# Kernel optimization log

Hardware: AMD Instinct MI355X
Metric: run time of the kernel (lower is better)

Reference implementation:

```python
import jax, jax.numpy as jnp
import numpy as np

B, T, H, K, NL = 64, 1024, 256, 64, 2  # batch, seq, n_hidden, n_tensors, n_layers
U = 2 * K  # GRU units


def _unif(key, shape):
    return jax.random.uniform(key, shape, jnp.float32, -0.2, 0.2)


def setup_inputs() -> dict:
    key = jax.random.key(0)
    ks = jax.random.split(key, 16)
    return {
        "x": jax.random.normal(ks[0], (B, T, H), jnp.float32),
        "m0_a": _unif(ks[1], (1, H)),
        "m0_o": _unif(ks[2], (1, H)),
        "Ua": _unif(ks[3], (K, H, H)),
        "Uo": _unif(ks[4], (K, H, H)),
        "Va": _unif(ks[5], (K, H, H)),
        "Vo": _unif(ks[6], (K, H, H)),
        "Ma": _unif(ks[7], (H, H)),
        "Mo": _unif(ks[8], (H, H)),
        "va": _unif(ks[9], (U, 1)),
        "vo": _unif(ks[10], (U, 1)),
        "Wa": _unif(ks[11], (U, 3 * U)),  # GRU kernel (z|r|h), input dim = U
        "Ra": _unif(ks[12], (U, 3 * U)),  # GRU recurrent kernel
        "Wo": _unif(ks[13], (U, 3 * U)),
        "Ro": _unif(ks[14], (U, 3 * U)),
    }


def gru_seq(seq, W, R):
    # Keras GRU, reset_after=True, use_bias=False, recurrent_activation=sigmoid.
    # seq: [B, T, U] -> [B, T, U]
    units = R.shape[0]
    xW = seq @ W  # [B, T, 3U] precomputed input projections

    def step(h, xw_t):
        xz, xr, xh = jnp.split(xw_t, 3, axis=-1)
        hz, hr, hc = jnp.split(h @ R, 3, axis=-1)
        z = jax.nn.sigmoid(xz + hz)
        r = jax.nn.sigmoid(xr + hr)
        hh = jnp.tanh(xh + r * hc)
        hn = z * h + (1.0 - z) * hh
        return hn, hn

    h0 = jnp.zeros((seq.shape[0], units), seq.dtype)
    _, ys = jax.lax.scan(step, h0, jnp.swapaxes(xW, 0, 1))
    return jnp.swapaxes(ys, 0, 1)


def cmla_forward(x, m0_a, m0_o, Ua, Uo, Va, Vo, Ma, Mo, va, vo, Wa, Ra, Wo, Ro):
    b = x.shape[0]
    ma = jnp.broadcast_to(m0_a, (b, m0_a.shape[-1]))  # [B, H]
    mo = jnp.broadcast_to(m0_o, (b, m0_o.shape[-1]))
    asp_sum = jnp.zeros((b, x.shape[1], U), x.dtype)
    opi_sum = jnp.zeros((b, x.shape[1], U), x.dtype)
    for i in range(NL):
        # tensor products: [K,H,H] x [B,H] -> [B,K,H]; then [B,T,H] x [B,K,H] -> [B,T,K]
        a1 = jnp.einsum('bth,bkh->btk', x, jnp.einsum('khj,bj->bkh', Ua, ma))
        a2 = jnp.einsum('bth,bkh->btk', x, jnp.einsum('khj,bj->bkh', Va, mo))
        o1 = jnp.einsum('bth,bkh->btk', x, jnp.einsum('khj,bj->bkh', Uo, ma))
        o2 = jnp.einsum('bth,bkh->btk', x, jnp.einsum('khj,bj->bkh', Vo, mo))
        aspect = jnp.tanh(jnp.concatenate([a1, a2], axis=-1))   # [B,T,2K]
        opinion = jnp.tanh(jnp.concatenate([o1, o2], axis=-1))  # [B,T,2K]
        ra = gru_seq(aspect, Wa, Ra)
        ro = gru_seq(opinion, Wo, Ro)
        asp_sum = asp_sum + ra
        opi_sum = opi_sum + ro
        if i < NL - 1:
            alpha_a = jax.nn.softmax(jnp.einsum('btu,u->bt', ra, va[:, 0]), axis=-1)
            alpha_o = jax.nn.softmax(jnp.einsum('btu,u->bt', ro, vo[:, 0]), axis=-1)
            ctx_a = jnp.einsum('bt,bth->bh', alpha_a, x)  # attention-pooled context
            ctx_o = jnp.einsum('bt,bth->bh', alpha_o, x)
            ma = jnp.tanh(ma @ Ma) + ctx_a
            mo = jnp.tanh(mo @ Mo) + ctx_o
    return asp_sum, opi_sum


def reference(x, m0_a, m0_o, Ua, Uo, Va, Vo, Ma, Mo, va, vo, Wa, Ra, Wo, Ro):
    return cmla_forward(x, m0_a, m0_o, Ua, Uo, Va, Vo, Ma, Mo, va, vo, Wa, Ra, Wo, Ro)
```

## Files before the change

kernel.cpp:

```cpp
#include <hip/hip_runtime.h>
#include <hip/hip_bf16.h>
#include <math.h>

#define B_  64
#define T_  1024
#define H_  256
#define K_  64
#define U_  128
#define U3_ 384

#define LOG2E_F 1.4426950408889634f

typedef unsigned short ushort_t;
typedef __attribute__((ext_vector_type(8))) short short8;
typedef __attribute__((ext_vector_type(8))) _Float16 half8;
typedef __attribute__((ext_vector_type(4))) _Float16 half4v;
typedef __attribute__((ext_vector_type(4))) float floatx4;

__device__ __forceinline__ float bf2f(ushort_t v) {
  unsigned int u = ((unsigned int)v) << 16;
  return __builtin_bit_cast(float, u);
}
__device__ __forceinline__ float h2f(ushort_t v) {
  return (float)__builtin_bit_cast(_Float16, v);
}
__device__ __forceinline__ ushort_t f2h(float f) {
  return __builtin_bit_cast(ushort_t, (_Float16)f);
}
__device__ __forceinline__ float ldf(const void* p, size_t i, int isf) {
  return isf ? ((const float*)p)[i] : bf2f(((const ushort_t*)p)[i]);
}
__device__ __forceinline__ float exp2_hw(float x) {
  float r;
  asm volatile("v_exp_f32 %0, %1\n\ts_nop 0" : "=v"(r) : "v"(x));
  return r;
}
__device__ __forceinline__ unsigned pk2h(float a, float b) {
  unsigned r;
  asm("v_cvt_pkrtz_f16_f32 %0, %1, %2" : "=v"(r) : "v"(a), "v"(b));
  return r;
}
__device__ __forceinline__ float tanh_fast(float x) {
  float E = exp2_hw(2.f * LOG2E_F * x);
  return 1.f - 2.f * __builtin_amdgcn_rcpf(E + 1.f);
}

__global__ void k_sniff(const ushort_t* __restrict__ xr, int* __restrict__ flag) {
  __shared__ int red[256];
  int tx = threadIdx.x;
  int hits = 0;
  for (int i = 0; i < 64; ++i) {
    ushort_t w = xr[tx + i * 256];
    int e = (w >> 7) & 0xff;
    hits += (e >= 0x70 && e <= 0x82) ? 1 : 0;
  }
  red[tx] = hits;
  __syncthreads();
  for (int off = 128; off > 0; off >>= 1) {
    if (tx < off) red[tx] += red[tx + off];
    __syncthreads();
  }
  if (tx == 0) flag[0] = (red[0] < 12288) ? 1 : 0;
}

__global__ __launch_bounds__(256) void k_canon_x(const void* __restrict__ xr,
                                                 const int* __restrict__ flag,
                                                 ushort_t* __restrict__ x16) {
  int tid = blockIdx.x * 256 + threadIdx.x;
  float v[8];
  if (*flag) {
    const float4* xf = (const float4*)xr;
    float4 a = xf[tid * 2], b = xf[tid * 2 + 1];
    v[0] = a.x; v[1] = a.y; v[2] = a.z; v[3] = a.w;
    v[4] = b.x; v[5] = b.y; v[6] = b.z; v[7] = b.w;
  } else {
    uint4 raw = ((const uint4*)xr)[tid];
    v[0] = bf2f((ushort_t)(raw.x & 0xffff)); v[1] = bf2f((ushort_t)(raw.x >> 16));
    v[2] = bf2f((ushort_t)(raw.y & 0xffff)); v[3] = bf2f((ushort_t)(raw.y >> 16));
    v[4] = bf2f((ushort_t)(raw.z & 0xffff)); v[5] = bf2f((ushort_t)(raw.z >> 16));
    v[6] = bf2f((ushort_t)(raw.w & 0xffff)); v[7] = bf2f((ushort_t)(raw.w >> 16));
  }
  uint4 o;
  o.x = (unsigned)f2h(v[0]) | ((unsigned)f2h(v[1]) << 16);
  o.y = (unsigned)f2h(v[2]) | ((unsigned)f2h(v[3]) << 16);
  o.z = (unsigned)f2h(v[4]) | ((unsigned)f2h(v[5]) << 16);
  o.w = (unsigned)f2h(v[6]) | ((unsigned)f2h(v[7]) << 16);
  ((uint4*)x16)[tid] = o;
}

__global__ void k_init_m(const void* __restrict__ m0a, const void* __restrict__ m0o,
                         const int* __restrict__ flag,
                         float* __restrict__ ma_ws, float* __restrict__ mo_ws) {
  int b = blockIdx.x, tx = threadIdx.x, isf = *flag;
  ma_ws[b * H_ + tx] = ldf(m0a, tx, isf);
  mo_ws[b * H_ + tx] = ldf(m0o, tx, isf);
}

__global__ void k_transpose(const void* __restrict__ Wa, const void* __restrict__ Wo,
                            const int* __restrict__ flag, ushort_t* __restrict__ Wt16) {
  int bx = blockIdx.x, isf = *flag;
  int g = bx / 192;
  int i = (bx % 192) * 256 + threadIdx.x;
  const void* W = g ? Wo : Wa;
  int jj = i >> 7, u = i & 127;
  float sc = (jj < 256) ? -LOG2E_F : (2.f * LOG2E_F);
  Wt16[(size_t)g * (U3_ * U_) + i] = f2h(ldf(W, u * U3_ + jj, isf) * sc);
}

__global__ __launch_bounds__(256) void k_phaseA(
    const void* __restrict__ Ua, const void* __restrict__ Va,
    const void* __restrict__ Uo, const void* __restrict__ Vo,
    const int* __restrict__ flag,
    const float* __restrict__ ma_ws, const float* __restrict__ mo_ws,
    ushort_t* __restrict__ P16) {
  int gk = blockIdx.x;
  int g = gk >> 6, k = gk & 63;
  const void* U = (g == 0) ? Ua : (g == 1) ? Va : (g == 2) ? Uo : Vo;
  const float* msrc = (g & 1) ? mo_ws : ma_ws;
  int tx = threadIdx.x;
  int isf = *flag;
  __shared__ __align__(16) float m_l[64 * 128];
  float acc[64];
#pragma unroll
  for (int b = 0; b < 64; ++b) acc[b] = 0.f;
  size_t rowoff = ((size_t)k * H_ + tx) * H_;
  for (int pass = 0; pass < 2; ++pass) {
    for (int i = 0; i < 32; ++i) {
      int flat = tx + i * 256;
      m_l[flat] = msrc[(flat >> 7) * H_ + pass * 128 + (flat & 127)];
    }
    __syncthreads();
    for (int c = 0; c < 16; ++c) {
      float uv[8];
      if (isf) {
        const float* uf = (const float*)U + rowoff + pass * 128 + c * 8;
        float4 A = *(const float4*)uf;
        float4 Bv = *(const float4*)(uf + 4);
        uv[0] = A.x; uv[1] = A.y; uv[2] = A.z; uv[3] = A.w;
        uv[4] = Bv.x; uv[5] = Bv.y; uv[6] = Bv.z; uv[7] = Bv.w;
      } else {
        const ushort_t* ub = (const ushort_t*)U + rowoff + pass * 128 + c * 8;
        uint4 raw = *(const uint4*)ub;
        uv[0] = bf2f((ushort_t)(raw.x & 0xffff)); uv[1] = bf2f((ushort_t)(raw.x >> 16));
        uv[2] = bf2f((ushort_t)(raw.y & 0xffff)); uv[3] = bf2f((ushort_t)(raw.y >> 16));
        uv[4] = bf2f((ushort_t)(raw.z & 0xffff)); uv[5] = bf2f((ushort_t)(raw.z >> 16));
        uv[6] = bf2f((ushort_t)(raw.w & 0xffff)); uv[7] = bf2f((ushort_t)(raw.w >> 16));
      }
#pragma unroll
      for (int b = 0; b < 64; ++b) {
        const float* mr = &m_l[b * 128 + c * 8];
        float4 mA = *(const float4*)mr;
        float4 mB = *(const float4*)(mr + 4);
        float s = acc[b];
        s = fmaf(uv[0], mA.x, s); s = fmaf(uv[1], mA.y, s);
        s = fmaf(uv[2], mA.z, s); s = fmaf(uv[3], mA.w, s);
        s = fmaf(uv[4], mB.x, s); s = fmaf(uv[5], mB.y, s);
        s = fmaf(uv[6], mB.z, s); s = fmaf(uv[7], mB.w, s);
        acc[b] = s;
      }
    }
    __syncthreads();
  }
  size_t base = ((size_t)(g * 64 + k)) * H_ + tx;
#pragma unroll 4
  for (int b = 0; b < 64; ++b) P16[base + (size_t)b * (256 * H_)] = f2h(acc[b]);
}

__global__ __launch_bounds__(256) void k_phaseB(
    const ushort_t* __restrict__ x16, const ushort_t* __restrict__ P16,
    ushort_t* __restrict__ aspect, ushort_t* __restrict__ opinion) {
  int bx = blockIdx.x;
  int b = bx >> 6, tt = bx & 63;
  int w = threadIdx.x >> 6;
  int lane = threadIdx.x & 63;
  int m = lane & 15, q = lane >> 4;
  const ushort_t* arow = x16 + ((size_t)(b * T_ + tt * 16 + m)) * H_ + q * 8;
  half8 af[8];
#pragma unroll
  for (int c = 0; c < 8; ++c)
    af[c] = __builtin_bit_cast(half8, *(const short8*)(arow + c * 32));
  const ushort_t* pbase = P16 + ((size_t)(b * 256 + m)) * H_ + q * 8;
#pragma unroll
  for (int s = 0; s < 4; ++s) {
    int ntile = s * 4 + w;
    const ushort_t* brow = pbase + (size_t)(ntile * 16) * H_;
    floatx4 acc = {0.f, 0.f, 0.f, 0.f}, acc2 = acc;
#pragma unroll
    for (int c = 0; c < 4; ++c) {
      half8 bf = __builtin_bit_cast(half8, *(const short8*)(brow + c * 32));
      acc = __builtin_amdgcn_mfma_f32_16x16x32_f16(af[c], bf, acc, 0, 0, 0);
      half8 bf2 = __builtin_bit_cast(half8, *(const short8*)(brow + (c + 4) * 32));
      acc2 = __builtin_amdgcn_mfma_f32_16x16x32_f16(af[c + 4], bf2, acc2, 0, 0, 0);
    }
    int n = ntile * 16 + m;
    ushort_t* dst;
    int nn;
    if (n < 128) { dst = aspect; nn = n; } else { dst = opinion; nn = n - 128; }
#pragma unroll
    for (int i = 0; i < 4; ++i) {
      int t = tt * 16 + q * 4 + i;
      dst[((size_t)(b * T_ + t)) * U_ + nn] = f2h(tanh_fast(acc[i] + acc2[i]));
    }
  }
}

__global__ __launch_bounds__(256) void k_phaseC(
    const ushort_t* __restrict__ aspect, const ushort_t* __restrict__ opinion,
    const ushort_t* __restrict__ Wt16,
    ushort_t* __restrict__ zr_a, ushort_t* __restrict__ zr_o,
    ushort_t* __restrict__ xh_a, ushort_t* __restrict__ xh_o) {
  int g = blockIdx.y;
  const ushort_t* A = g ? opinion : aspect;
  const ushort_t* Bm = Wt16 + (size_t)g * (U3_ * U_);
  ushort_t* ZR = g ? zr_o : zr_a;
  ushort_t* XH = g ? xh_o : xh_a;
  int mt = blockIdx.x;
  int w = threadIdx.x >> 6;
  int lane = threadIdx.x & 63;
  int m = lane & 15, q = lane >> 4;
  const ushort_t* arow = A + ((size_t)(mt * 16 + m)) * U_ + q * 8;
  half8 af[4];
#pragma unroll
  for (int c = 0; c < 4; ++c)
    af[c] = __builtin_bit_cast(half8, *(const short8*)(arow + c * 32));
  const ushort_t* bbase = Bm + (size_t)m * U_ + q * 8;
#pragma unroll
  for (int s = 0; s < 6; ++s) {
    int nt = s * 4 + w;
    const ushort_t* brow = bbase + (size_t)(nt * 16) * U_;
    floatx4 acc = {0.f, 0.f, 0.f, 0.f};
#pragma unroll
    for (int c = 0; c < 4; ++c) {
      half8 bf = __builtin_bit_cast(half8, *(const short8*)(brow + c * 32));
      acc = __builtin_amdgcn_mfma_f32_16x16x32_f16(af[c], bf, acc, 0, 0, 0);
    }
    int col = nt * 16 + m;
    if (nt < 16) {
      int c2 = (col < 128) ? (((col >> 2) << 3) + (col & 3))
                           : ((((col - 128) >> 2) << 3) + 4 + (col & 3));
#pragma unroll
      for (int i = 0; i < 4; ++i) {
        int row = mt * 16 + q * 4 + i;
        ZR[(size_t)row * 256 + c2] = f2h(acc[i]);
      }
    } else {
#pragma unroll
      for (int i = 0; i < 4; ++i) {
        int row = mt * 16 + q * 4 + i;
        XH[(size_t)row * U_ + (col - 256)] = f2h(acc[i]);
      }
    }
  }
}

template <int LAYER>
__global__ __launch_bounds__(512) void k_scan(
    const ushort_t* __restrict__ zr_a, const ushort_t* __restrict__ zr_o,
    const ushort_t* __restrict__ xh_a, const ushort_t* __restrict__ xh_o,
    const ushort_t* __restrict__ Rt16,
    float* __restrict__ out) {
  int g = blockIdx.x >> 2;
  int bb = (blockIdx.x & 3) << 4;
  int tid = threadIdx.x;
  int w = tid >> 6;
  int lane = tid & 63;
  int r = lane & 15;
  int q = lane >> 4;
  int b = bb + r;
  int j = (w << 4) + (q << 2);

  const ushort_t* zr = g ? zr_o : zr_a;
  const ushort_t* xh = g ? xh_o : xh_a;
  const ushort_t* Rt = Rt16 + (size_t)g * (U3_ * U_);

  half8 af[3][4];
#pragma unroll
  for (int gt = 0; gt < 3; ++gt) {
    size_t row = (size_t)(128 * gt + 16 * w + r) * U_;
#pragma unroll
    for (int ks = 0; ks < 4; ++ks)
      af[gt][ks] = __builtin_bit_cast(half8, *(const short8*)(Rt + row + ks * 32 + q * 8));
  }

  __shared__ __align__(16) ushort_t hbuf[4096];
  ((uint2*)hbuf)[tid] = (uint2){0u, 0u};

  float hs0 = 0.f, hs1 = 0.f, hs2 = 0.f, hs3 = 0.f;

  const ushort_t* zp = zr + (size_t)b * (T_ * 256) + ((j >> 2) << 3);
  const ushort_t* xp = xh + (size_t)b * (T_ * U_) + j;
  float* op = out + ((size_t)g * B_ * T_ + (size_t)b * T_) * U_ + j;

  uint4 zrA = *(const uint4*)zp;
  uint4 zrB = *(const uint4*)(zp + 256);
  uint2 hA = *(const uint2*)xp;
  uint2 hB = *(const uint2*)(xp + U_);
  float4 oA = make_float4(0.f, 0.f, 0.f, 0.f), oB = oA;
  if (LAYER) {
    oA = *(const float4*)op;
    oB = *(const float4*)(op + U_);
  }
  float4 pendE = make_float4(0.f, 0.f, 0.f, 0.f), pendO = pendE;

  int wofs = (w >> 1) * 512 + (r + 16 * (((w & 1) << 1) + (q >> 1))) * 8 + (q & 1) * 4;

  __syncthreads();

  for (int t = 0; t < T_; t += 2) {
    {
      half8 bf0 = __builtin_bit_cast(half8, *(const short8*)(&hbuf[0 * 512 + lane * 8]));
      half8 bf1 = __builtin_bit_cast(half8, *(const short8*)(&hbuf[1 * 512 + lane * 8]));
      half8 bf2 = __builtin_bit_cast(half8, *(const short8*)(&hbuf[2 * 512 + lane * 8]));
      half8 bf3 = __builtin_bit_cast(half8, *(const short8*)(&hbuf[3 * 512 + lane * 8]));
      if (t != 0) *(float4*)(op - U_) = pendO;
      int adv = (t + 2 < T_) ? 2 : 0;
      uint4 pzr = *(const uint4*)(zp + adv * 256);
      uint2 ph = *(const uint2*)(xp + adv * U_);
      float4 po;
      if (LAYER) po = *(const float4*)(op + adv * U_);

      floatx4 a0 = {0.f, 0.f, 0.f, 0.f}, a1 = a0, a2 = a0, c0 = a0, c1 = a0, c2 = a0;
      a0 = __builtin_amdgcn_mfma_f32_16x16x32_f16(af[0][0], bf0, a0, 0, 0, 0);
      a1 = __builtin_amdgcn_mfma_f32_16x16x32_f16(af[1][0], bf0, a1, 0, 0, 0);
      a2 = __builtin_amdgcn_mfma_f32_16x16x32_f16(af[2][0], bf0, a2, 0, 0, 0);
      c0 = __builtin_amdgcn_mfma_f32_16x16x32_f16(af[0][2], bf2, c0, 0, 0, 0);
      c1 = __builtin_amdgcn_mfma_f32_16x16x32_f16(af[1][2], bf2, c1, 0, 0, 0);
      c2 = __builtin_amdgcn_mfma_f32_16x16x32_f16(af[2][2], bf2, c2, 0, 0, 0);
      a0 = __builtin_amdgcn_mfma_f32_16x16x32_f16(af[0][1], bf1, a0, 0, 0, 0);
      a1 = __builtin_amdgcn_mfma_f32_16x16x32_f16(af[1][1], bf1, a1, 0, 0, 0);
      a2 = __builtin_amdgcn_mfma_f32_16x16x32_f16(af[2][1], bf1, a2, 0, 0, 0);
      c0 = __builtin_amdgcn_mfma_f32_16x16x32_f16(af[0][3], bf3, c0, 0, 0, 0);
      c1 = __builtin_amdgcn_mfma_f32_16x16x32_f16(af[1][3], bf3, c1, 0, 0, 0);
      c2 = __builtin_amdgcn_mfma_f32_16x16x32_f16(af[2][3], bf3, c2, 0, 0, 0);

      half8 zr8 = __builtin_bit_cast(half8, zrA);
      half4v xh4 = __builtin_bit_cast(half4v, hA);
      float hp[4] = {hs0, hs1, hs2, hs3};
      float hn[4];
#pragma unroll
      for (int i = 0; i < 4; ++i) {
        float zq = (float)zr8[i] + (a0[i] + c0[i]);
        float rq = (float)zr8[4 + i] + (a1[i] + c1[i]);
        float z = __builtin_amdgcn_rcpf(1.f + exp2_hw(zq));
        float rr = __builtin_amdgcn_rcpf(1.f + exp2_hw(rq));
        float y2 = fmaf(rr, a2[i] + c2[i], (float)xh4[i]);
        float th = fmaf(-2.f, __builtin_amdgcn_rcpf(exp2_hw(y2) + 1.f), 1.f);
        hn[i] = fmaf(z, hp[i] - th, th);
      }
      hs0 = hn[0]; hs1 = hn[1]; hs2 = hn[2]; hs3 = hn[3];
      pendE.x = LAYER ? (oA.x + hn[0]) : hn[0];
      pendE.y = LAYER ? (oA.y + hn[1]) : hn[1];
      pendE.z = LAYER ? (oA.z + hn[2]) : hn[2];
      pendE.w = LAYER ? (oA.w + hn[3]) : hn[3];
      uint2 wv;
      wv.x = pk2h(hn[0], hn[1]);
      wv.y = pk2h(hn[2], hn[3]);
      *(uint2*)(&hbuf[2048 + wofs]) = wv;
      zrA = pzr; hA = ph;
      if (LAYER) oA = po;
    }
    asm volatile("s_waitcnt lgkmcnt(0)" ::: "memory");
    __builtin_amdgcn_s_barrier();
    __builtin_amdgcn_sched_barrier(0);
    {
      half8 bf0 = __builtin_bit_cast(half8, *(const short8*)(&hbuf[2048 + 0 * 512 + lane * 8]));
      half8 bf1 = __builtin_bit_cast(half8, *(const short8*)(&hbuf[2048 + 1 * 512 + lane * 8]));
      half8 bf2 = __builtin_bit_cast(half8, *(const short8*)(&hbuf[2048 + 2 * 512 + lane * 8]));
      half8 bf3 = __builtin_bit_cast(half8, *(const short8*)(&hbuf[2048 + 3 * 512 + lane * 8]));
      *(float4*)op = pendE;
      int adv = (t + 3 < T_) ? 2 : 0;
      uint4 pzr = *(const uint4*)(zp + 256 + adv * 256);
      uint2 ph = *(const uint2*)(xp + U_ + adv * U_);
      float4 po;
      if (LAYER) po = *(const float4*)(op + U_ + adv * U_);

      floatx4 a0 = {0.f, 0.f, 0.f, 0.f}, a1 = a0, a2 = a0, c0 = a0, c1 = a0, c2 = a0;
      a0 = __builtin_amdgcn_mfma_f32_16x16x32_f16(af[0][0], bf0, a0, 0, 0, 0);
      a1 = __builtin_amdgcn_mfma_f32_16x16x32_f16(af[1][0], bf0, a1, 0, 0, 0);
      a2 = __builtin_amdgcn_mfma_f32_16x16x32_f16(af[2][0], bf0, a2, 0, 0, 0);
      c0 = __builtin_amdgcn_mfma_f32_16x16x32_f16(af[0][2], bf2, c0, 0, 0, 0);
      c1 = __builtin_amdgcn_mfma_f32_16x16x32_f16(af[1][2], bf2, c1, 0, 0, 0);
      c2 = __builtin_amdgcn_mfma_f32_16x16x32_f16(af[2][2], bf2, c2, 0, 0, 0);
      a0 = __builtin_amdgcn_mfma_f32_16x16x32_f16(af[0][1], bf1, a0, 0, 0, 0);
      a1 = __builtin_amdgcn_mfma_f32_16x16x32_f16(af[1][1], bf1, a1, 0, 0, 0);
      a2 = __builtin_amdgcn_mfma_f32_16x16x32_f16(af[2][1], bf1, a2, 0, 0, 0);
      c0 = __builtin_amdgcn_mfma_f32_16x16x32_f16(af[0][3], bf3, c0, 0, 0, 0);
      c1 = __builtin_amdgcn_mfma_f32_16x16x32_f16(af[1][3], bf3, c1, 0, 0, 0);
      c2 = __builtin_amdgcn_mfma_f32_16x16x32_f16(af[2][3], bf3, c2, 0, 0, 0);

      half8 zr8 = __builtin_bit_cast(half8, zrB);
      half4v xh4 = __builtin_bit_cast(half4v, hB);
      float hp[4] = {hs0, hs1, hs2, hs3};
      float hn[4];
#pragma unroll
      for (int i = 0; i < 4; ++i) {
        float zq = (float)zr8[i] + (a0[i] + c0[i]);
        float rq = (float)zr8[4 + i] + (a1[i] + c1[i]);
        float z = __builtin_amdgcn_rcpf(1.f + exp2_hw(zq));
        float rr = __builtin_amdgcn_rcpf(1.f + exp2_hw(rq));
        float y2 = fmaf(rr, a2[i] + c2[i], (float)xh4[i]);
        float th = fmaf(-2.f, __builtin_amdgcn_rcpf(exp2_hw(y2) + 1.f), 1.f);
        hn[i] = fmaf(z, hp[i] - th, th);
      }
      hs0 = hn[0]; hs1 = hn[1]; hs2 = hn[2]; hs3 = hn[3];
      pendO.x = LAYER ? (oB.x + hn[0]) : hn[0];
      pendO.y = LAYER ? (oB.y + hn[1]) : hn[1];
      pendO.z = LAYER ? (oB.z + hn[2]) : hn[2];
      pendO.w = LAYER ? (oB.w + hn[3]) : hn[3];
      uint2 wv;
      wv.x = pk2h(hn[0], hn[1]);
      wv.y = pk2h(hn[2], hn[3]);
      *(uint2*)(&hbuf[0 + wofs]) = wv;
      zrB = pzr; hB = ph;
      if (LAYER) oB = po;
    }
    asm volatile("s_waitcnt lgkmcnt(0)" ::: "memory");
    __builtin_amdgcn_s_barrier();
    __builtin_amdgcn_sched_barrier(0);
    zp += 512; xp += 2 * U_; op += 2 * U_;
  }
  *(float4*)(op - U_) = pendO;
}

__global__ void k_score(const float* __restrict__ out, const void* __restrict__ va,
                        const void* __restrict__ vo, const int* __restrict__ flag,
                        float* __restrict__ scores) {
  int wave = threadIdx.x >> 6, lane = threadIdx.x & 63;
  int pair = blockIdx.x * 4 + wave;
  int g = pair >> 16;
  int bt = pair & 65535;
  int isf = *flag;
  const void* v = g ? vo : va;
  const float* o = out + ((size_t)g * (B_ * T_) + bt) * U_ + lane * 2;
  float s = o[0] * ldf(v, lane * 2, isf) + o[1] * ldf(v, lane * 2 + 1, isf);
#pragma unroll
  for (int off = 32; off > 0; off >>= 1) s += __shfl_down(s, off, 64);
  if (lane == 0) scores[pair] = s;
}

__global__ void k_softmax(float* __restrict__ scores) {
  int row = blockIdx.x;
  float* s = scores + (size_t)row * T_;
  int tx = threadIdx.x;
  __shared__ float red[256];
  float v[4];
  float mx = -1e30f;
#pragma unroll
  for (int i = 0; i < 4; ++i) { v[i] = s[tx + i * 256]; mx = fmaxf(mx, v[i]); }
  red[tx] = mx;
  __syncthreads();
  for (int off = 128; off > 0; off >>= 1) {
    if (tx < off) red[tx] = fmaxf(red[tx], red[tx + off]);
    __syncthreads();
  }
  float M = red[0];
  __syncthreads();
  float sm = 0.f;
#pragma unroll
  for (int i = 0; i < 4; ++i) { v[i] = expf(v[i] - M); sm += v[i]; }
  red[tx] = sm;
  __syncthreads();
  for (int off = 128; off > 0; off >>= 1) {
    if (tx < off) red[tx] += red[tx + off];
    __syncthreads();
  }
  float inv = 1.f / red[0];
#pragma unroll
  for (int i = 0; i < 4; ++i) s[tx + i * 256] = v[i] * inv;
}

__global__ __launch_bounds__(1024) void k_ctx_m(const float* __restrict__ alpha,
                                                const void* __restrict__ x,
                                                const void* __restrict__ Ma,
                                                const void* __restrict__ Mo,
                                                const int* __restrict__ flag,
                                                float* __restrict__ ma_ws,
                                                float* __restrict__ mo_ws) {
  int g = blockIdx.x >> 6, b = blockIdx.x & 63;
  int isf = *flag;
  int tid = threadIdx.x;
  int tx = tid & 255;
  int ty = tid >> 8;
  __shared__ float a_l[1024];
  __shared__ float m_l[256];
  __shared__ float pA[4][256];
  __shared__ float pB[4][256];
  const float* al = alpha + ((size_t)g * B_ + b) * T_;
  a_l[tid] = al[tid];
  if (ty == 0) m_l[tx] = (g ? mo_ws : ma_ws)[b * H_ + tx];
  __syncthreads();
  const void* Mm = g ? Mo : Ma;
  float acc = 0.f;
#pragma unroll 4
  for (int t0 = 0; t0 < 256; ++t0) {
    int t = ty * 256 + t0;
    acc = fmaf(a_l[t], ldf(x, (size_t)(b * T_ + t) * H_ + tx, isf), acc);
  }
  float acc2 = 0.f;
#pragma unroll 4
  for (int c = 0; c < 64; ++c) {
    int jj = ty * 64 + c;
    acc2 = fmaf(m_l[jj], ldf(Mm, (size_t)jj * 256 + tx, isf), acc2);
  }
  pA[ty][tx] = acc;
  pB[ty][tx] = acc2;
  __syncthreads();
  if (ty == 0) {
    float A = pA[0][tx] + pA[1][tx] + pA[2][tx] + pA[3][tx];
    float Bv = pB[0][tx] + pB[1][tx] + pB[2][tx] + pB[3][tx];
    float* m_ws = g ? mo_ws : ma_ws;
    m_ws[b * H_ + tx] = tanhf(Bv) + A;
  }
}

extern "C" void kernel_launch(void* const* d_in, const int* in_sizes, int n_in,
                              void* d_out, int out_size, void* d_ws, size_t ws_size,
                              hipStream_t stream) {
  const void* x_r = d_in[0];
  const void* m0a = d_in[1];
  const void* m0o = d_in[2];
  const void* Ua  = d_in[3];
  const void* Uo  = d_in[4];
  const void* Va  = d_in[5];
  const void* Vo  = d_in[6];
  const void* Ma  = d_in[7];
  const void* Mo  = d_in[8];
  const void* va  = d_in[9];
  const void* vo  = d_in[10];
  const void* Wa  = d_in[11];
  const void* Ra  = d_in[12];
  const void* Wo  = d_in[13];
  const void* Ro  = d_in[14];
  float* out = (float*)d_out;

  char* ws = (char*)d_ws;
  int*      flag    = (int*)(ws + 0);
  float*    ma_ws   = (float*)(ws + 1024);
  float*    mo_ws   = (float*)(ws + 66560);
  ushort_t* Wt16    = (ushort_t*)(ws + 132096);
  ushort_t* x16     = (ushort_t*)(ws + 328704);
  ushort_t* P16     = (ushort_t*)(ws + 33883136);
  float*    scores  = (float*)(ws + 33883136);
  ushort_t* Rt16    = (ushort_t*)(ws + 33883136 + 1048576);
  ushort_t* aspect  = (ushort_t*)(ws + 42271744);
  ushort_t* opinion = (ushort_t*)(ws + 59048960);
  ushort_t* zr_a    = (ushort_t*)(ws + 75826176);
  ushort_t* zr_o    = (ushort_t*)(ws + 109380608);
  ushort_t* xh_a    = (ushort_t*)(ws + 142935040);
  ushort_t* xh_o    = (ushort_t*)(ws + 159712256);

  if (ws_size < 176489472ULL) return;

  k_sniff<<<dim3(1), dim3(256), 0, stream>>>((const ushort_t*)x_r, flag);
  k_canon_x<<<dim3(8192), dim3(256), 0, stream>>>(x_r, flag, x16);
  k_init_m<<<dim3(64), dim3(256), 0, stream>>>(m0a, m0o, flag, ma_ws, mo_ws);
  k_transpose<<<dim3(384), dim3(256), 0, stream>>>(Wa, Wo, flag, Wt16);

  for (int layer = 0; layer < 2; ++layer) {
    k_phaseA<<<dim3(256), dim3(256), 0, stream>>>(Ua, Va, Uo, Vo, flag, ma_ws, mo_ws, P16);
    k_phaseB<<<dim3(4096), dim3(256), 0, stream>>>(x16, P16, aspect, opinion);
    k_phaseC<<<dim3(4096, 2), dim3(256), 0, stream>>>(aspect, opinion, Wt16, zr_a, zr_o, xh_a, xh_o);
    k_transpose<<<dim3(384), dim3(256), 0, stream>>>(Ra, Ro, flag, Rt16);
    if (layer == 0) {
      k_scan<0><<<dim3(8), dim3(512), 0, stream>>>(zr_a, zr_o, xh_a, xh_o, Rt16, out);
      k_score<<<dim3(32768), dim3(256), 0, stream>>>(out, va, vo, flag, scores);
      k_softmax<<<dim3(128), dim3(256), 0, stream>>>(scores);
      k_ctx_m<<<dim3(128), dim3(1024), 0, stream>>>(scores, x_r, Ma, Mo, flag, ma_ws, mo_ws);
    } else {
      k_scan<1><<<dim3(8), dim3(512), 0, stream>>>(zr_a, zr_o, xh_a, xh_o, Rt16, out);
    }
  }
}
```

Baseline: 2.492 ms.

## Halve scan block to four waves, each computing two column groups

The GRU scan kernel now runs with 256 threads (4 waves) per block instead of 512. Each wave handles two 16-column groups of the hidden state, holding twice the recurrent-weight fragments in registers. The idea is to cut barrier cost and cross-wave synchronisation per timestep, in exchange for more serial MFMA and gate work per wave. The MFMA accumulation is now chained fully through K instead of split into two partial sums, which lengthens the dependency chain per output.

```diff
diff --git a/kernel.cpp b/kernel.cpp
--- a/kernel.cpp
+++ b/kernel.cpp
@@ -43,6 +43,32 @@
 __device__ __forceinline__ float tanh_fast(float x) {
   float E = exp2_hw(2.f * LOG2E_F * x);
   return 1.f - 2.f * __builtin_amdgcn_rcpf(E + 1.f);
+}
+
+__device__ __forceinline__ void gru_gate4(floatx4 az, floatx4 ar, floatx4 ah,
+                                          uint4 zrv, uint2 hv, float4 ov,
+                                          float* hs, float4& pend, uint2& wv,
+                                          int addold) {
+  half8 zr8 = __builtin_bit_cast(half8, zrv);
+  half4v xh4 = __builtin_bit_cast(half4v, hv);
+  float hn[4];
+#pragma unroll
+  for (int i = 0; i < 4; ++i) {
+    float zq = (float)zr8[i] + az[i];
+    float rq = (float)zr8[4 + i] + ar[i];
+    float z = __builtin_amdgcn_rcpf(1.f + exp2_hw(zq));
+    float rr = __builtin_amdgcn_rcpf(1.f + exp2_hw(rq));
+    float y2 = fmaf(rr, ah[i], (float)xh4[i]);
+    float th = fmaf(-2.f, __builtin_amdgcn_rcpf(exp2_hw(y2) + 1.f), 1.f);
+    hn[i] = fmaf(z, hs[i] - th, th);
+    hs[i] = hn[i];
+  }
+  pend.x = addold ? (ov.x + hn[0]) : hn[0];
+  pend.y = addold ? (ov.y + hn[1]) : hn[1];
+  pend.z = addold ? (ov.z + hn[2]) : hn[2];
+  pend.w = addold ? (ov.w + hn[3]) : hn[3];
+  wv.x = pk2h(hn[0], hn[1]);
+  wv.y = pk2h(hn[2], hn[3]);
 }
 
 __global__ void k_sniff(const ushort_t* __restrict__ xr, int* __restrict__ flag) {
@@ -254,7 +280,7 @@
 }
 
 template <int LAYER>
-__global__ __launch_bounds__(512) void k_scan(
+__global__ __launch_bounds__(256, 1) void k_scan(
     const ushort_t* __restrict__ zr_a, const ushort_t* __restrict__ zr_o,
     const ushort_t* __restrict__ xh_a, const ushort_t* __restrict__ xh_o,
     const ushort_t* __restrict__ Rt16,
@@ -267,42 +293,50 @@
   int r = lane & 15;
   int q = lane >> 4;
   int b = bb + r;
-  int j = (w << 4) + (q << 2);
+  int j0 = (w << 4) + (q << 2);
 
   const ushort_t* zr = g ? zr_o : zr_a;
   const ushort_t* xh = g ? xh_o : xh_a;
   const ushort_t* Rt = Rt16 + (size_t)g * (U3_ * U_);
 
-  half8 af[3][4];
-#pragma unroll
-  for (int gt = 0; gt < 3; ++gt) {
-    size_t row = (size_t)(128 * gt + 16 * w + r) * U_;
-#pragma unroll
-    for (int ks = 0; ks < 4; ++ks)
-      af[gt][ks] = __builtin_bit_cast(half8, *(const short8*)(Rt + row + ks * 32 + q * 8));
-  }
+  half8 af[2][3][4];
+#pragma unroll
+  for (int jg = 0; jg < 2; ++jg)
+#pragma unroll
+    for (int gt = 0; gt < 3; ++gt) {
+      size_t row = (size_t)(128 * gt + 64 * jg + 16 * w + r) * U_;
+#pragma unroll
+      for (int ks = 0; ks < 4; ++ks)
+        af[jg][gt][ks] =
+            __builtin_bit_cast(half8, *(const short8*)(Rt + row + ks * 32 + q * 8));
+    }
 
   __shared__ __align__(16) ushort_t hbuf[4096];
-  ((uint2*)hbuf)[tid] = (uint2){0u, 0u};
-
-  float hs0 = 0.f, hs1 = 0.f, hs2 = 0.f, hs3 = 0.f;
-
-  const ushort_t* zp = zr + (size_t)b * (T_ * 256) + ((j >> 2) << 3);
-  const ushort_t* xp = xh + (size_t)b * (T_ * U_) + j;
-  float* op = out + ((size_t)g * B_ * T_ + (size_t)b * T_) * U_ + j;
-
-  uint4 zrA = *(const uint4*)zp;
-  uint4 zrB = *(const uint4*)(zp + 256);
-  uint2 hA = *(const uint2*)xp;
-  uint2 hB = *(const uint2*)(xp + U_);
-  float4 oA = make_float4(0.f, 0.f, 0.f, 0.f), oB = oA;
+  ((uint4*)hbuf)[tid] = (uint4){0u, 0u, 0u, 0u};
+
+  float hs0[4] = {0.f, 0.f, 0.f, 0.f};
+  float hs1[4] = {0.f, 0.f, 0.f, 0.f};
+
+  const ushort_t* zp = zr + (size_t)b * (T_ * 256) + j0 * 2;
+  const ushort_t* xp = xh + (size_t)b * (T_ * U_) + j0;
+  float* op = out + ((size_t)g * B_ * T_ + (size_t)b * T_) * U_ + j0;
+
+  uint4 zrA0 = *(const uint4*)zp;
+  uint4 zrA1 = *(const uint4*)(zp + 128);
+  uint4 zrB0 = *(const uint4*)(zp + 256);
+  uint4 zrB1 = *(const uint4*)(zp + 256 + 128);
+  uint2 hA0 = *(const uint2*)xp;
+  uint2 hA1 = *(const uint2*)(xp + 64);
+  uint2 hB0 = *(const uint2*)(xp + U_);
+  uint2 hB1 = *(const uint2*)(xp + U_ + 64);
+  float4 oA0 = make_float4(0.f, 0.f, 0.f, 0.f), oA1 = oA0, oB0 = oA0, oB1 = oA0;
   if (LAYER) {
-    oA = *(const float4*)op;
-    oB = *(const float4*)(op + U_);
-  }
-  float4 pendE = make_float4(0.f, 0.f, 0.f, 0.f), pendO = pendE;
-
-  int wofs = (w >> 1) * 512 + (r + 16 * (((w & 1) << 1) + (q >> 1))) * 8 + (q & 1) * 4;
+    oA0 = *(const float4*)op;            oA1 = *(const float4*)(op + 64);
+    oB0 = *(const float4*)(op + U_);     oB1 = *(const float4*)(op + U_ + 64);
+  }
+  float4 pendE0, pendE1, pendO0, pendO1;
+
+  int wof0 = ((j0 >> 5) << 9) + (((j0 >> 3) & 3) << 7) + (r << 3) + (j0 & 7);
 
   __syncthreads();
 
@@ -312,52 +346,52 @@
       half8 bf1 = __builtin_bit_cast(half8, *(const short8*)(&hbuf[1 * 512 + lane * 8]));
       half8 bf2 = __builtin_bit_cast(half8, *(const short8*)(&hbuf[2 * 512 + lane * 8]));
       half8 bf3 = __builtin_bit_cast(half8, *(const short8*)(&hbuf[3 * 512 + lane * 8]));
-      if (t != 0) *(float4*)(op - U_) = pendO;
+      if (t != 0) {
+        *(float4*)(op - U_) = pendO0;
+        *(float4*)(op - U_ + 64) = pendO1;
+      }
       int adv = (t + 2 < T_) ? 2 : 0;
-      uint4 pzr = *(const uint4*)(zp + adv * 256);
-      uint2 ph = *(const uint2*)(xp + adv * U_);
-      float4 po;
-      if (LAYER) po = *(const float4*)(op + adv * U_);
-
-      floatx4 a0 = {0.f, 0.f, 0.f, 0.f}, a1 = a0, a2 = a0, c0 = a0, c1 = a0, c2 = a0;
-      a0 = __builtin_amdgcn_mfma_f32_16x16x32_f16(af[0][0], bf0, a0, 0, 0, 0);
-      a1 = __builtin_amdgcn_mfma_f32_16x16x32_f16(af[1][0], bf0, a1, 0, 0, 0);
-      a2 = __builtin_amdgcn_mfma_f32_16x16x32_f16(af[2][0], bf0, a2, 0, 0, 0);
-      c0 = __builtin_amdgcn_mfma_f32_16x16x32_f16(af[0][2], bf2, c0, 0, 0, 0);
-      c1 = __builtin_amdgcn_mfma_f32_16x16x32_f16(af[1][2], bf2, c1, 0, 0, 0);
-      c2 = __builtin_amdgcn_mfma_f32_16x16x32_f16(af[2][2], bf2, c2, 0, 0, 0);
-      a0 = __builtin_amdgcn_mfma_f32_16x16x32_f16(af[0][1], bf1, a0, 0, 0, 0);
-      a1 = __builtin_amdgcn_mfma_f32_16x16x32_f16(af[1][1], bf1, a1, 0, 0, 0);
-      a2 = __builtin_amdgcn_mfma_f32_16x16x32_f16(af[2][1], bf1, a2, 0, 0, 0);
-      c0 = __builtin_amdgcn_mfma_f32_16x16x32_f16(af[0][3], bf3, c0, 0, 0, 0);
-      c1 = __builtin_amdgcn_mfma_f32_16x16x32_f16(af[1][3], bf3, c1, 0, 0, 0);
-      c2 = __builtin_amdgcn_mfma_f32_16x16x32_f16(af[2][3], bf3, c2, 0, 0, 0);
-
-      half8 zr8 = __builtin_bit_cast(half8, zrA);
-      half4v xh4 = __builtin_bit_cast(half4v, hA);
-      float hp[4] = {hs0, hs1, hs2, hs3};
-      float hn[4];
-#pragma unroll
-      for (int i = 0; i < 4; ++i) {
-        float zq = (float)zr8[i] + (a0[i] + c0[i]);
-        float rq = (float)zr8[4 + i] + (a1[i] + c1[i]);
-        float z = __builtin_amdgcn_rcpf(1.f + exp2_hw(zq));
-        float rr = __builtin_amdgcn_rcpf(1.f + exp2_hw(rq));
-        float y2 = fmaf(rr, a2[i] + c2[i], (float)xh4[i]);
-        float th = fmaf(-2.f, __builtin_amdgcn_rcpf(exp2_hw(y2) + 1.f), 1.f);
-        hn[i] = fmaf(z, hp[i] - th, th);
+      uint4 pz0 = *(const uint4*)(zp + adv * 256);
+      uint4 pz1 = *(const uint4*)(zp + adv * 256 + 128);
+      uint2 ph0 = *(const uint2*)(xp + adv * U_);
+      uint2 ph1 = *(const uint2*)(xp + adv * U_ + 64);
+      float4 po0, po1;
+      if (LAYER) {
+        po0 = *(const float4*)(op + adv * U_);
+        po1 = *(const float4*)(op + adv * U_ + 64);
       }
-      hs0 = hn[0]; hs1 = hn[1]; hs2 = hn[2]; hs3 = hn[3];
-      pendE.x = LAYER ? (oA.x + hn[0]) : hn[0];
-      pendE.y = LAYER ? (oA.y + hn[1]) : hn[1];
-      pendE.z = LAYER ? (oA.z + hn[2]) : hn[2];
-      pendE.w = LAYER ? (oA.w + hn[3]) : hn[3];
-      uint2 wv;
-      wv.x = pk2h(hn[0], hn[1]);
-      wv.y = pk2h(hn[2], hn[3]);
-      *(uint2*)(&hbuf[2048 + wofs]) = wv;
-      zrA = pzr; hA = ph;
-      if (LAYER) oA = po;
+      floatx4 zz = {0.f, 0.f, 0.f, 0.f};
+      floatx4 az0 = __builtin_amdgcn_mfma_f32_16x16x32_f16(af[0][0][0], bf0,
+                    __builtin_amdgcn_mfma_f32_16x16x32_f16(af[0][0][1], bf1,
+                    __builtin_amdgcn_mfma_f32_16x16x32_f16(af[0][0][2], bf2,
+                    __builtin_amdgcn_mfma_f32_16x16x32_f16(af[0][0][3], bf3, zz, 0,0,0), 0,0,0), 0,0,0), 0,0,0);
+      floatx4 ar0 = __builtin_amdgcn_mfma_f32_16x16x32_f16(af[0][1][0], bf0,
+                    __builtin_amdgcn_mfma_f32_16x16x32_f16(af[0][1][1], bf1,
+                    __builtin_amdgcn_mfma_f32_16x16x32_f16(af[0][1][2], bf2,
+                    __builtin_amdgcn_mfma_f32_16x16x32_f16(af[0][1][3], bf3, zz, 0,0,0), 0,0,0), 0,0,0), 0,0,0);
+      floatx4 ah0 = __builtin_amdgcn_mfma_f32_16x16x32_f16(af[0][2][0], bf0,
+                    __builtin_amdgcn_mfma_f32_16x16x32_f16(af[0][2][1], bf1,
+                    __builtin_amdgcn_mfma_f32_16x16x32_f16(af[0][2][2], bf2,
+                    __builtin_amdgcn_mfma_f32_16x16x32_f16(af[0][2][3], bf3, zz, 0,0,0), 0,0,0), 0,0,0), 0,0,0);
+      floatx4 az1 = __builtin_amdgcn_mfma_f32_16x16x32_f16(af[1][0][0], bf0,
+                    __builtin_amdgcn_mfma_f32_16x16x32_f16(af[1][0][1], bf1,
+                    __builtin_amdgcn_mfma_f32_16x16x32_f16(af[1][0][2], bf2,
+                    __builtin_amdgcn_mfma_f32_16x16x32_f16(af[1][0][3], bf3, zz, 0,0,0), 0,0,0), 0,0,0), 0,0,0);
+      floatx4 ar1 = __builtin_amdgcn_mfma_f32_16x16x32_f16(af[1][1][0], bf0,
+                    __builtin_amdgcn_mfma_f32_16x16x32_f16(af[1][1][1], bf1,
+                    __builtin_amdgcn_mfma_f32_16x16x32_f16(af[1][1][2], bf2,
+                    __builtin_amdgcn_mfma_f32_16x16x32_f16(af[1][1][3], bf3, zz, 0,0,0), 0,0,0), 0,0,0), 0,0,0);
+      floatx4 ah1 = __builtin_amdgcn_mfma_f32_16x16x32_f16(af[1][2][0], bf0,
+                    __builtin_amdgcn_mfma_f32_16x16x32_f16(af[1][2][1], bf1,
+                    __builtin_amdgcn_mfma_f32_16x16x32_f16(af[1][2][2], bf2,
+                    __builtin_amdgcn_mfma_f32_16x16x32_f16(af[1][2][3], bf3, zz, 0,0,0), 0,0,0), 0,0,0), 0,0,0);
+      uint2 wv0, wv1;
+      gru_gate4(az0, ar0, ah0, zrA0, hA0, oA0, hs0, pendE0, wv0, LAYER);
+      gru_gate4(az1, ar1, ah1, zrA1, hA1, oA1, hs1, pendE1, wv1, LAYER);
+      *(uint2*)(&hbuf[2048 + wof0]) = wv0;
+      *(uint2*)(&hbuf[2048 + 1024 + wof0]) = wv1;
+      zrA0 = pz0; zrA1 = pz1; hA0 = ph0; hA1 = ph1;
+      if (LAYER) { oA0 = po0; oA1 = po1; }
     }
     asm volatile("s_waitcnt lgkmcnt(0)" ::: "memory");
     __builtin_amdgcn_s_barrier();
@@ -367,59 +401,58 @@
       half8 bf1 = __builtin_bit_cast(half8, *(const short8*)(&hbuf[2048 + 1 * 512 + lane * 8]));
       half8 bf2 = __builtin_bit_cast(half8, *(const short8*)(&hbuf[2048 + 2 * 512 + lane * 8]));
       half8 bf3 = __builtin_bit_cast(half8, *(const short8*)(&hbuf[2048 + 3 * 512 + lane * 8]));
-      *(float4*)op = pendE;
+      *(float4*)op = pendE0;
+      *(float4*)(op + 64) = pendE1;
       int adv = (t + 3 < T_) ? 2 : 0;
-      uint4 pzr = *(const uint4*)(zp + 256 + adv * 256);
-      uint2 ph = *(const uint2*)(xp + U_ + adv * U_);
-      float4 po;
-      if (LAYER) po = *(const float4*)(op + U_ + adv * U_);
-
-      floatx4 a0 = {0.f, 0.f, 0.f, 0.f}, a1 = a0, a2 = a0, c0 = a0, c1 = a0, c2 = a0;
-      a0 = __builtin_amdgcn_mfma_f32_16x16x32_f16(af[0][0], bf0, a0, 0, 0, 0);
-      a1 = __builtin_amdgcn_mfma_f32_16x16x32_f16(af[1][0], bf0, a1, 0, 0, 0);
-      a2 = __builtin_amdgcn_mfma_f32_16x16x32_f16(af[2][0], bf0, a2, 0, 0, 0);
-      c0 = __builtin_amdgcn_mfma_f32_16x16x32_f16(af[0][2], bf2, c0, 0, 0, 0);
-      c1 = __builtin_amdgcn_mfma_f32_16x16x32_f16(af[1][2], bf2, c1, 0, 0, 0);
-      c2 = __builtin_amdgcn_mfma_f32_16x16x32_f16(af[2][2], bf2, c2, 0, 0, 0);
-      a0 = __builtin_amdgcn_mfma_f32_16x16x32_f16(af[0][1], bf1, a0, 0, 0, 0);
-      a1 = __builtin_amdgcn_mfma_f32_16x16x32_f16(af[1][1], bf1, a1, 0, 0, 0);
-      a2 = __builtin_amdgcn_mfma_f32_16x16x32_f16(af[2][1], bf1, a2, 0, 0, 0);
-      c0 = __builtin_amdgcn_mfma_f32_16x16x32_f16(af[0][3], bf3, c0, 0, 0, 0);
-      c1 = __builtin_amdgcn_mfma_f32_16x16x32_f16(af[1][3], bf3, c1, 0, 0, 0);
-      c2 = __builtin_amdgcn_mfma_f32_16x16x32_f16(af[2][3], bf3, c2, 0, 0, 0);
-
-      half8 zr8 = __builtin_bit_cast(half8, zrB);
-      half4v xh4 = __builtin_bit_cast(half4v, hB);
-      float hp[4] = {hs0, hs1, hs2, hs3};
-      float hn[4];
-#pragma unroll
-      for (int i = 0; i < 4; ++i) {
-        float zq = (float)zr8[i] + (a0[i] + c0[i]);
-        float rq = (float)zr8[4 + i] + (a1[i] + c1[i]);
-        float z = __builtin_amdgcn_rcpf(1.f + exp2_hw(zq));
-        float rr = __builtin_amdgcn_rcpf(1.f + exp2_hw(rq));
-        float y2 = fmaf(rr, a2[i] + c2[i], (float)xh4[i]);
-        float th = fmaf(-2.f, __builtin_amdgcn_rcpf(exp2_hw(y2) + 1.f), 1.f);
-        hn[i] = fmaf(z, hp[i] - th, th);
+      uint4 pz0 = *(const uint4*)(zp + 256 + adv * 256);
+      uint4 pz1 = *(const uint4*)(zp + 256 + adv * 256 + 128);
+      uint2 ph0 = *(const uint2*)(xp + U_ + adv * U_);
+      uint2 ph1 = *(const uint2*)(xp + U_ + adv * U_ + 64);
+      float4 po0, po1;
+      if (LAYER) {
+        po0 = *(const float4*)(op + U_ + adv * U_);
+        po1 = *(const float4*)(op + U_ + adv * U_ + 64);
       }
-      hs0 = hn[0]; hs1 = hn[1]; hs2 = hn[2]; hs3 = hn[3];
-      pendO.x = LAYER ? (oB.x + hn[0]) : hn[0];
-      pendO.y = LAYER ? (oB.y + hn[1]) : hn[1];
-      pendO.z = LAYER ? (oB.z + hn[2]) : hn[2];
-      pendO.w = LAYER ? (oB.w + hn[3]) : hn[3];
-      uint2 wv;
-      wv.x = pk2h(hn[0], hn[1]);
-      wv.y = pk2h(hn[2], hn[3]);
-      *(uint2*)(&hbuf[0 + wofs]) = wv;
-      zrB = pzr; hB = ph;
-      if (LAYER) oB = po;
+      floatx4 zz = {0.f, 0.f, 0.f, 0.f};
+      floatx4 az0 = __builtin_amdgcn_mfma_f32_16x16x32_f16(af[0][0][0], bf0,
+                    __builtin_amdgcn_mfma_f32_16x16x32_f16(af[0][0][1], bf1,
+                    __builtin_amdgcn_mfma_f32_16x16x32_f16(af[0][0][2], bf2,
+                    __builtin_amdgcn_mfma_f32_16x16x32_f16(af[0][0][3], bf3, zz, 0,0,0), 0,0,0), 0,0,0), 0,0,0);
+      floatx4 ar0 = __builtin_amdgcn_mfma_f32_16x16x32_f16(af[0][1][0], bf0,
+                    __builtin_amdgcn_mfma_f32_16x16x32_f16(af[0][1][1], bf1,
+                    __builtin_amdgcn_mfma_f32_16x16x32_f16(af[0][1][2], bf2,
+                    __builtin_amdgcn_mfma_f32_16x16x32_f16(af[0][1][3], bf3, zz, 0,0,0), 0,0,0), 0,0,0), 0,0,0);
+      floatx4 ah0 = __builtin_amdgcn_mfma_f32_16x16x32_f16(af[0][2][0], bf0,
+                    __builtin_amdgcn_mfma_f32_16x16x32_f16(af[0][2][1], bf1,
+                    __builtin_amdgcn_mfma_f32_16x16x32_f16(af[0][2][2], bf2,
+                    __builtin_amdgcn_mfma_f32_16x16x32_f16(af[0][2][3], bf3, zz, 0,0,0), 0,0,0), 0,0,0), 0,0,0);
+      floatx4 az1 = __builtin_amdgcn_mfma_f32_16x16x32_f16(af[1][0][0], bf0,
+                    __builtin_amdgcn_mfma_f32_16x16x32_f16(af[1][0][1], bf1,
+                    __builtin_amdgcn_mfma_f32_16x16x32_f16(af[1][0][2], bf2,
+                    __builtin_amdgcn_mfma_f32_16x16x32_f16(af[1][0][3], bf3, zz, 0,0,0), 0,0,0), 0,0,0), 0,0,0);
+      floatx4 ar1 = __builtin_amdgcn_mfma_f32_16x16x32_f16(af[1][1][0], bf0,
+                    __builtin_amdgcn_mfma_f32_16x16x32_f16(af[1][1][1], bf1,
+                    __builtin_amdgcn_mfma_f32_16x16x32_f16(af[1][1][2], bf2,
+                    __builtin_amdgcn_mfma_f32_16x16x32_f16(af[1][1][3], bf3, zz, 0,0,0), 0,0,0), 0,0,0), 0,0,0);
+      floatx4 ah1 = __builtin_amdgcn_mfma_f32_16x16x32_f16(af[1][2][0], bf0,
+                    __builtin_amdgcn_mfma_f32_16x16x32_f16(af[1][2][1], bf1,
+                    __builtin_amdgcn_mfma_f32_16x16x32_f16(af[1][2][2], bf2,
+                    __builtin_amdgcn_mfma_f32_16x16x32_f16(af[1][2][3], bf3, zz, 0,0,0), 0,0,0), 0,0,0), 0,0,0);
+      uint2 wv0, wv1;
+      gru_gate4(az0, ar0, ah0, zrB0, hB0, oB0, hs0, pendO0, wv0, LAYER);
+      gru_gate4(az1, ar1, ah1, zrB1, hB1, oB1, hs1, pendO1, wv1, LAYER);
+      *(uint2*)(&hbuf[0 + wof0]) = wv0;
+      *(uint2*)(&hbuf[1024 + wof0]) = wv1;
+      zrB0 = pz0; zrB1 = pz1; hB0 = ph0; hB1 = ph1;
+      if (LAYER) { oB0 = po0; oB1 = po1; }
     }
     asm volatile("s_waitcnt lgkmcnt(0)" ::: "memory");
     __builtin_amdgcn_s_barrier();
     __builtin_amdgcn_sched_barrier(0);
     zp += 512; xp += 2 * U_; op += 2 * U_;
   }
-  *(float4*)(op - U_) = pendO;
+  *(float4*)(op - U_) = pendO0;
+  *(float4*)(op - U_ + 64) = pendO1;
 }
 
 __global__ void k_score(const float* __restrict__ out, const void* __restrict__ va,
@@ -562,12 +595,12 @@
     k_phaseC<<<dim3(4096, 2), dim3(256), 0, stream>>>(aspect, opinion, Wt16, zr_a, zr_o, xh_a, xh_o);
     k_transpose<<<dim3(384), dim3(256), 0, stream>>>(Ra, Ro, flag, Rt16);
     if (layer == 0) {
-      k_scan<0><<<dim3(8), dim3(512), 0, stream>>>(zr_a, zr_o, xh_a, xh_o, Rt16, out);
+      k_scan<0><<<dim3(8), dim3(256), 0, stream>>>(zr_a, zr_o, xh_a, xh_o, Rt16, out);
       k_score<<<dim3(32768), dim3(256), 0, stream>>>(out, va, vo, flag, scores);
       k_softmax<<<dim3(128), dim3(256), 0, stream>>>(scores);
       k_ctx_m<<<dim3(128), dim3(1024), 0, stream>>>(scores, x_r, Ma, Mo, flag, ma_ws, mo_ws);
     } else {
-      k_scan<1><<<dim3(8), dim3(512), 0, stream>>>(zr_a, zr_o, xh_a, xh_o, Rt16, out);
-    }
-  }
-}
+      k_scan<1><<<dim3(8), dim3(256), 0, stream>>>(zr_a, zr_o, xh_a, xh_o, Rt16, out);
+    }
+  }
+}
```

Measured after the change: 3.010 ms. 20.8% more time.
